# Optimization experiments

Measured on AMD Instinct MI355X. Metric: run time of the kernel, lower is better.

Reference implementation:

```python
import jax, jax.numpy as jnp
import numpy as np

N_BITS = 8
QMAX = float(2 ** (N_BITS - 1) - 1)   # 127
QMIN = -QMAX - 1.0                     # -128
EPS = 1e-8


def _fq(x, scale):
    # symmetric fake quant: round, clamp, dequant
    return jnp.clip(jnp.round(x / scale), QMIN, QMAX) * scale


def fake_quant_per_token(x):
    # one scale per [..., :] vector (amax over last dim)
    max_abs = jnp.max(jnp.abs(x), axis=-1, keepdims=True)
    scale = jnp.maximum(max_abs / QMAX, EPS)
    return _fq(x, scale)


def fake_quant_per_channel(w):
    # w: [out, in]; ch_axis=0 -> one scale per output row (reduce over dim 1)
    max_abs = jnp.max(jnp.abs(w), axis=1, keepdims=True)
    scale = jnp.maximum(max_abs / QMAX, EPS)
    return _fq(w, scale)


def setup_inputs() -> dict:
    key = jax.random.key(0)
    kx, kw, kb = jax.random.split(key, 3)
    B, S, D_IN, D_OUT = 4, 2048, 4096, 4096
    x = jax.random.normal(kx, (B, S, D_IN), dtype=jnp.float32)
    w = jax.random.normal(kw, (D_OUT, D_IN), dtype=jnp.float32) * 0.02
    b = jax.random.normal(kb, (D_OUT,), dtype=jnp.float32) * 0.02
    return {"x": x, "w": w, "b": b}


def reference(x, w, b):
    # fake-quant path: W8 per-channel weight, A8 per-token activation
    w_q = fake_quant_per_channel(w)           # [O, I]
    x_q = fake_quant_per_token(x)             # [B, S, I]
    y = jnp.einsum('bsi,oi->bso', x_q, w_q) + b
    return y
```

## Files before the change

### kernel.cpp

```cpp
#include <hip/hip_runtime.h>
#include <hip/hip_bf16.h>


#define K_DIM 4096
#define N_DIM 4096

typedef int v4i __attribute__((ext_vector_type(4)));

__device__ __forceinline__ void cp16(void* lds, const void* g) {
    __builtin_amdgcn_global_load_lds(
        (const __attribute__((address_space(1))) void*)g,
        (__attribute__((address_space(3))) void*)lds, 16, 0, 0);
}

__global__ __launch_bounds__(256) void quant_rows_kernel(
    const float* __restrict__ x, const float* __restrict__ w, int M,
    char* __restrict__ qx, char* __restrict__ qw,
    float* __restrict__ sx, float* __restrict__ sw) {
    const int blk = blockIdx.x;
    const bool is_x = blk < M;
    const int row = is_x ? blk : blk - M;
    const float* rp = (is_x ? x : w) + (size_t)row * 4096;
    char* qdst = is_x ? qx : qw;
    float* sdst = is_x ? sx : sw;

    const int tid = threadIdx.x;

    float4 v[4];
#pragma unroll
    for (int i = 0; i < 4; ++i)
        v[i] = *(const float4*)(rp + 4 * (tid + 256 * i));

    float m = 0.0f;
#pragma unroll
    for (int i = 0; i < 4; ++i) {
        m = fmaxf(m, fmaxf(fmaxf(fabsf(v[i].x), fabsf(v[i].y)),
                           fmaxf(fabsf(v[i].z), fabsf(v[i].w))));
    }
#pragma unroll
    for (int off = 32; off > 0; off >>= 1)
        m = fmaxf(m, __shfl_down(m, off));

    __shared__ float red[4];
    if ((tid & 63) == 0) red[tid >> 6] = m;
    __syncthreads();
    const float amax = fmaxf(fmaxf(red[0], red[1]), fmaxf(red[2], red[3]));
    const float scale = fmaxf(amax / 127.0f, 1e-8f);

    int* qout = (int*)(qdst + (size_t)row * 4096);
#pragma unroll
    for (int i = 0; i < 4; ++i) {
        int q0 = (int)fminf(fmaxf(rintf(v[i].x / scale), -128.0f), 127.0f);
        int q1 = (int)fminf(fmaxf(rintf(v[i].y / scale), -128.0f), 127.0f);
        int q2 = (int)fminf(fmaxf(rintf(v[i].z / scale), -128.0f), 127.0f);
        int q3 = (int)fminf(fmaxf(rintf(v[i].w / scale), -128.0f), 127.0f);
        qout[tid + 256 * i] =
            (q0 & 255) | ((q1 & 255) << 8) | ((q2 & 255) << 16) | ((q3 & 255) << 24);
    }
    if (tid == 0) sdst[row] = scale;
}

__global__ __launch_bounds__(256) void gemm_i8_kernel(
    const char* __restrict__ qx, const char* __restrict__ qw,
    const float* __restrict__ sx, const float* __restrict__ sw,
    const float* __restrict__ bias, float* __restrict__ y) {

    __shared__ __align__(16) char As[128 * 64];
    __shared__ __align__(16) char Bs[128 * 64];

    const int tid = threadIdx.x;
    const int wave = tid >> 6;
    const int lane = tid & 63;
    const int ln = lane & 15;
    const int lg = lane >> 4;
    const int wm = wave & 1;
    const int wn = wave >> 1;

    const int bm = blockIdx.y;
    const int bn = blockIdx.x;

    const char* aBase = qx + (size_t)bm * 128 * K_DIM;
    const char* bBase = qw + (size_t)bn * 128 * K_DIM;

    const int c0 = tid;
    const int c1 = tid + 256;
    const int r0 = c0 >> 2;
    const int r1 = c1 >> 2;
    const int kc0 = (c0 & 3) ^ ((c0 >> 3) & 3);
    const int kc1 = (c1 & 3) ^ ((c1 >> 3) & 3);

    v4i acc[4][4] = {};

    const int kxor = (lg ^ ((ln >> 1) & 3)) << 4;
    int aOff[4], bOff[4];
#pragma unroll
    for (int t = 0; t < 4; ++t) {
        aOff[t] = (wm * 64 + t * 16 + ln) * 64 + kxor;
        bOff[t] = (wn * 64 + t * 16 + ln) * 64 + kxor;
    }

    for (int k0 = 0; k0 < K_DIM; k0 += 64) {
        cp16(As + c0 * 16, aBase + (size_t)r0 * K_DIM + k0 + kc0 * 16);
        cp16(As + c1 * 16, aBase + (size_t)r1 * K_DIM + k0 + kc1 * 16);
        cp16(Bs + c0 * 16, bBase + (size_t)r0 * K_DIM + k0 + kc0 * 16);
        cp16(Bs + c1 * 16, bBase + (size_t)r1 * K_DIM + k0 + kc1 * 16);
        __syncthreads();

        v4i afr[4], bfr[4];
#pragma unroll
        for (int t = 0; t < 4; ++t) afr[t] = *(const v4i*)(As + aOff[t]);
#pragma unroll
        for (int t = 0; t < 4; ++t) bfr[t] = *(const v4i*)(Bs + bOff[t]);

#pragma unroll
        for (int mt = 0; mt < 4; ++mt)
#pragma unroll
            for (int nt = 0; nt < 4; ++nt)
                acc[mt][nt] = __builtin_amdgcn_mfma_i32_16x16x64_i8(
                    afr[mt], bfr[nt], acc[mt][nt], 0, 0, 0);

        __syncthreads();
    }

    const int m_base = bm * 128 + wm * 64;
    const int n_base = bn * 128 + wn * 64;

    float sxr[4][4];
#pragma unroll
    for (int mt = 0; mt < 4; ++mt)
#pragma unroll
        for (int r = 0; r < 4; ++r)
            sxr[mt][r] = sx[m_base + mt * 16 + lg * 4 + r];

#pragma unroll
    for (int nt = 0; nt < 4; ++nt) {
        const int n = n_base + nt * 16 + ln;
        const float swv = sw[n];
        const float bv = bias[n];
#pragma unroll
        for (int mt = 0; mt < 4; ++mt) {
            const int row = m_base + mt * 16 + lg * 4;
#pragma unroll
            for (int r = 0; r < 4; ++r) {
                y[(size_t)(row + r) * N_DIM + n] =
                    (float)acc[mt][nt][r] * sxr[mt][r] * swv + bv;
            }
        }
    }
}

extern "C" void kernel_launch(void* const* d_in, const int* in_sizes, int n_in,
                              void* d_out, int out_size, void* d_ws, size_t ws_size,
                              hipStream_t stream) {
    const float* x = (const float*)d_in[0];
    const float* w = (const float*)d_in[1];
    const float* b = (const float*)d_in[2];
    float* y = (float*)d_out;

    const int M = in_sizes[0] / K_DIM;
    const int O = in_sizes[1] / K_DIM;

    char* qx = (char*)d_ws;
    char* qw = qx + (size_t)M * K_DIM;
    float* sx = (float*)(qw + (size_t)O * K_DIM);
    float* sw = sx + M;

    quant_rows_kernel<<<M + O, 256, 0, stream>>>(x, w, M, qx, qw, sx, sw);

    dim3 grid(N_DIM / 128, M / 128);
    gemm_i8_kernel<<<grid, 256, 0, stream>>>(qx, qw, sx, sw, b, y);
}
```

Measured before the change: 429.8 us.

## Double-buffer LDS tiles to overlap global loads with MFMA compute

Splits the shared-memory A/B tiles into two buffers and issues the asynchronous global-to-LDS copy for the next K slice before computing on the current one. The loop is unrolled by two with one barrier per slice instead of two, so load latency can hide behind the int8 MFMA work. It doubles LDS use per block, which may lower occupancy. The last iteration issues a redundant wrap-around prefetch of slice zero that is never consumed.

```diff
diff --git a/kernel.cpp b/kernel.cpp
--- a/kernel.cpp
+++ b/kernel.cpp
@@ -65,8 +65,8 @@
     const float* __restrict__ sx, const float* __restrict__ sw,
     const float* __restrict__ bias, float* __restrict__ y) {
 
-    __shared__ __align__(16) char As[128 * 64];
-    __shared__ __align__(16) char Bs[128 * 64];
+    __shared__ __align__(16) char As[2][128 * 64];
+    __shared__ __align__(16) char Bs[2][128 * 64];
 
     const int tid = threadIdx.x;
     const int wave = tid >> 6;
@@ -89,6 +89,14 @@
     const int kc0 = (c0 & 3) ^ ((c0 >> 3) & 3);
     const int kc1 = (c1 & 3) ^ ((c1 >> 3) & 3);
 
+#define STAGE(buf, kk)                                                        \
+    do {                                                                      \
+        cp16(As[buf] + c0 * 16, aBase + (size_t)r0 * K_DIM + (kk) + kc0 * 16);\
+        cp16(As[buf] + c1 * 16, aBase + (size_t)r1 * K_DIM + (kk) + kc1 * 16);\
+        cp16(Bs[buf] + c0 * 16, bBase + (size_t)r0 * K_DIM + (kk) + kc0 * 16);\
+        cp16(Bs[buf] + c1 * 16, bBase + (size_t)r1 * K_DIM + (kk) + kc1 * 16);\
+    } while (0)
+
     v4i acc[4][4] = {};
 
     const int kxor = (lg ^ ((ln >> 1) & 3)) << 4;
@@ -99,27 +107,32 @@
         bOff[t] = (wn * 64 + t * 16 + ln) * 64 + kxor;
     }
 
-    for (int k0 = 0; k0 < K_DIM; k0 += 64) {
-        cp16(As + c0 * 16, aBase + (size_t)r0 * K_DIM + k0 + kc0 * 16);
-        cp16(As + c1 * 16, aBase + (size_t)r1 * K_DIM + k0 + kc1 * 16);
-        cp16(Bs + c0 * 16, bBase + (size_t)r0 * K_DIM + k0 + kc0 * 16);
-        cp16(Bs + c1 * 16, bBase + (size_t)r1 * K_DIM + k0 + kc1 * 16);
+#define COMPUTE(buf)                                                          \
+    do {                                                                      \
+        v4i afr[4], bfr[4];                                                   \
+        _Pragma("unroll")                                                     \
+        for (int t = 0; t < 4; ++t) afr[t] = *(const v4i*)(As[buf] + aOff[t]);\
+        _Pragma("unroll")                                                     \
+        for (int t = 0; t < 4; ++t) bfr[t] = *(const v4i*)(Bs[buf] + bOff[t]);\
+        _Pragma("unroll")                                                     \
+        for (int mt = 0; mt < 4; ++mt)                                        \
+            _Pragma("unroll")                                                 \
+            for (int nt = 0; nt < 4; ++nt)                                    \
+                acc[mt][nt] = __builtin_amdgcn_mfma_i32_16x16x64_i8(          \
+                    afr[mt], bfr[nt], acc[mt][nt], 0, 0, 0);                  \
+    } while (0)
+
+    STAGE(0, 0);
+
+    for (int k0 = 0; k0 < K_DIM; k0 += 128) {
         __syncthreads();
-
-        v4i afr[4], bfr[4];
-#pragma unroll
-        for (int t = 0; t < 4; ++t) afr[t] = *(const v4i*)(As + aOff[t]);
-#pragma unroll
-        for (int t = 0; t < 4; ++t) bfr[t] = *(const v4i*)(Bs + bOff[t]);
-
-#pragma unroll
-        for (int mt = 0; mt < 4; ++mt)
-#pragma unroll
-            for (int nt = 0; nt < 4; ++nt)
-                acc[mt][nt] = __builtin_amdgcn_mfma_i32_16x16x64_i8(
-                    afr[mt], bfr[nt], acc[mt][nt], 0, 0, 0);
+        STAGE(1, k0 + 64);
+        COMPUTE(0);
 
         __syncthreads();
+        const int kn = (k0 + 128) & (K_DIM - 1);
+        STAGE(0, kn);
+        COMPUTE(1);
     }
 
     const int m_base = bm * 128 + wm * 64;
```

Result: slower. 450.0 us (+4.7%).
